# Kernel tuning notes

Hardware: AMD Instinct MI355X
Metric: run time of the kernel (lower is better)

## Reference

```python
import jax, jax.numpy as jnp
import numpy as np

NEG_SLOPE = 0.01  # torch leaky_relu default

def _leaky_relu(x):
    return jnp.where(x >= 0, x, NEG_SLOPE * x)

def setup_inputs() -> dict:
    key = jax.random.key(0)
    ks = jax.random.split(key, 12)
    n_drug, n_disease, n_edges, d = 10000, 10000, 1000000, 100
    inp = {
        "x_drug": jax.random.normal(ks[0], (n_drug, d), dtype=jnp.float32),
        "x_disease": jax.random.normal(ks[1], (n_disease, d), dtype=jnp.float32),
        "edge_label_index": jax.random.randint(ks[2], (2, n_edges), 0, n_drug, dtype=jnp.int64),
        "W1": jax.random.normal(ks[3], (200, 128), dtype=jnp.float32) * 0.07,
        "b1": jax.random.normal(ks[4], (128,), dtype=jnp.float32) * 0.01,
        "W2": jax.random.normal(ks[5], (128, 32), dtype=jnp.float32) * 0.09,
        "b2": jax.random.normal(ks[6], (32,), dtype=jnp.float32) * 0.01,
        "W3": jax.random.normal(ks[7], (32, 16), dtype=jnp.float32) * 0.18,
        "b3": jax.random.normal(ks[8], (16,), dtype=jnp.float32) * 0.01,
        "W4": jax.random.normal(ks[9], (16, 1), dtype=jnp.float32) * 0.25,
        "b4": jax.random.normal(ks[10], (1,), dtype=jnp.float32) * 0.01,
    }
    return inp

def reference(x_drug, x_disease, edge_label_index, W1, b1, W2, b2, W3, b3, W4, b4):
    # gather per-edge node embeddings and concat -> [E, 200]
    ef = jnp.concatenate([x_drug[edge_label_index[0]],
                          x_disease[edge_label_index[1]]], axis=-1)
    ef = _leaky_relu(ef @ W1 + b1)
    ef = _leaky_relu(ef @ W2 + b2)
    ef = _leaky_relu(ef @ W3 + b3)
    ef = ef @ W4 + b4
    return jnp.squeeze(ef, axis=-1)
```

## Files before the change

### kernel.cpp

```cpp
#include <hip/hip_runtime.h>
#include <cstdint>
#include <cstddef>

typedef _Float16 hf2   __attribute__((ext_vector_type(2)));
typedef _Float16 f16x8 __attribute__((ext_vector_type(8)));
typedef float    f32x4 __attribute__((ext_vector_type(4)));

__device__ __forceinline__ f16x8 q2h8(uint4 q) { union { uint4 q; f16x8 h; } c; c.q = q; return c.h; }
__device__ __forceinline__ hf2 pkrtz(float lo, float hi) {
    auto v = __builtin_amdgcn_cvt_pkrtz(lo, hi);
    union { decltype(v) a; hf2 b; } c; c.a = v; return c.b;
}
__device__ __forceinline__ float lreluf(float x) { return fmaxf(x, 0.01f * x); }
__device__ __forceinline__ f16x8 lrelu8(uint4 a, uint4 b) {
    f16x8 s = q2h8(a) + q2h8(b);
    f16x8 m = s * (_Float16)0.01f;
    return __builtin_elementwise_max(s, m);
}

__global__ __launch_bounds__(256) void node_proj2(
    const float* __restrict__ xd, const float* __restrict__ xi,
    const float* __restrict__ W1, const float* __restrict__ b1,
    _Float16* __restrict__ Pd, _Float16* __restrict__ Pi,
    int nd, int ni, int nblk_d, int nblk_i,
    const float* __restrict__ W2, const float* __restrict__ W3,
    _Float16* __restrict__ W2f, _Float16* __restrict__ W3f,
    const unsigned* __restrict__ ew, long long nwords, int* __restrict__ flag)
{
    const int t = threadIdx.x;
    const int nproj = nblk_d + nblk_i;

    if ((int)blockIdx.x >= nproj) {
        if ((int)blockIdx.x == nproj) {
            for (int idx = t; idx < 4096; idx += 256) {
                int i  = idx & 7;
                int l  = (idx >> 3) & 63;
                int kt = (idx >> 9) & 3;
                int nt = (idx >> 11) & 1;
                int k = kt * 32 + 8 * (l >> 4) + i;
                int j = nt * 16 + (l & 15);
                W2f[idx] = (_Float16)W2[k * 32 + j];
            }
            for (int idx = t; idx < 512; idx += 256) {
                int i = idx & 7, l = idx >> 3;
                W3f[idx] = (_Float16)W3[(8 * (l >> 4) + i) * 16 + (l & 15)];
            }
        } else if (t < 64) {
            const long long pairs = nwords / 2;
            const long long step  = pairs / 64;
            unsigned v = 0;
            for (int s = 0; s < 4; ++s) {
                long long p = (long long)t * step + (long long)s * (step / 4 + 1);
                if (p < pairs) v |= ew[2 * p + 1];
            }
            unsigned long long ball = __ballot(v != 0);
            if (t == 0) *flag = (ball == 0ULL) ? 1 : 0;
        }
        return;
    }

    __shared__ float xs[1600];
    const int c  = t & 127;
    const int ty = t >> 7;
    const bool dis = (int)blockIdx.x >= nblk_d;
    const int b = dis ? (blockIdx.x - nblk_d) : blockIdx.x;
    const int n = dis ? ni : nd;
    const float* x = dis ? xi : xd;
    const float* W = dis ? (W1 + 100 * 128) : W1;
    _Float16* P = dis ? Pi : Pd;
    const float bv = dis ? b1[c] : 0.f;
    const int r0 = b * 16;

    const long long gbase = (long long)r0 * 100;
    const long long lim   = (long long)n * 100;
    for (int idx = t; idx < 1600; idx += 256) {
        long long g = gbase + idx;
        xs[idx] = (g < lim) ? x[g] : 0.f;
    }
    __syncthreads();

    float acc[8];
#pragma unroll
    for (int i = 0; i < 8; ++i) acc[i] = bv;

    const float4* xs4 = (const float4*)xs;
#pragma unroll 5
    for (int kk = 0; kk < 25; ++kk) {
        float w0 = W[(4 * kk + 0) * 128 + c];
        float w1 = W[(4 * kk + 1) * 128 + c];
        float w2 = W[(4 * kk + 2) * 128 + c];
        float w3 = W[(4 * kk + 3) * 128 + c];
#pragma unroll
        for (int i = 0; i < 8; ++i) {
            float4 xv = xs4[(ty * 8 + i) * 25 + kk];
            acc[i] = fmaf(xv.x, w0, acc[i]);
            acc[i] = fmaf(xv.y, w1, acc[i]);
            acc[i] = fmaf(xv.z, w2, acc[i]);
            acc[i] = fmaf(xv.w, w3, acc[i]);
        }
    }
#pragma unroll
    for (int i = 0; i < 8; ++i) {
        int r = r0 + ty * 8 + i;
        if (r < n) P[(size_t)r * 128 + c] = (_Float16)acc[i];
    }
}

__global__ __launch_bounds__(64, 4) void edge_mlp(
    const void* __restrict__ eidx_raw,
    const _Float16* __restrict__ Pd, const _Float16* __restrict__ Pi,
    const _Float16* __restrict__ W2f, const float* __restrict__ b2,
    const _Float16* __restrict__ W3f, const float* __restrict__ b3,
    const float* __restrict__ W4, const float* __restrict__ b4,
    const int* __restrict__ flag64,
    float* __restrict__ out, int E)
{
    __shared__ __align__(16) float H2[64 * 36];

    const int l  = threadIdx.x;
    const int er = l & 15;
    const int cg = l >> 4;
    const int base = blockIdx.x * 64;
    const int e_c = min(base + l, E - 1);

    int i0, i1;
    if (*flag64) {
        const long long* p = (const long long*)eidx_raw;
        i0 = (int)p[e_c];
        i1 = (int)p[(size_t)E + e_c];
    } else {
        const int* p = (const int*)eidx_raw;
        i0 = p[e_c];
        i1 = p[(size_t)E + e_c];
    }

    f16x8 bf0[4], bf1[4];
    {
        const uint4* W2q = (const uint4*)W2f;
#pragma unroll
        for (int kt = 0; kt < 4; ++kt) {
            bf0[kt] = q2h8(W2q[kt * 64 + l]);
            bf1[kt] = q2h8(W2q[256 + kt * 64 + l]);
        }
    }
    const f16x8 w3f = q2h8(((const uint4*)W3f)[l]);
    const float  b2v0 = b2[er], b2v1 = b2[16 + er];
    const float4 b3q  = ((const float4*)b3)[cg];
    const float4 w4q  = ((const float4*)W4)[cg];
    const float  b4v  = b4[0];

#pragma unroll
    for (int q = 0; q < 4; ++q) {
        const int src = q * 16 + er;
        const int j0 = __shfl(i0, src, 64);
        const int j1 = __shfl(i1, src, 64);
        const uint4* rowD = (const uint4*)(Pd + (size_t)j0 * 128);
        const uint4* rowI = (const uint4*)(Pi + (size_t)j1 * 128);

        f32x4 c0 = {0.f, 0.f, 0.f, 0.f}, c1 = {0.f, 0.f, 0.f, 0.f};
#pragma unroll
        for (int kt = 0; kt < 4; ++kt) {
            f16x8 af = lrelu8(rowD[kt * 4 + cg], rowI[kt * 4 + cg]);
            c0 = __builtin_amdgcn_mfma_f32_16x16x32_f16(af, bf0[kt], c0, 0, 0, 0);
            c1 = __builtin_amdgcn_mfma_f32_16x16x32_f16(af, bf1[kt], c1, 0, 0, 0);
        }

#pragma unroll
        for (int r = 0; r < 4; ++r) {
            const int e = q * 16 + 4 * cg + r;
            H2[e * 36 + er]      = lreluf(c0[r] + b2v0);
            H2[e * 36 + 16 + er] = lreluf(c1[r] + b2v1);
        }
        __syncthreads();

        const int e2 = q * 16 + er;
        const float4* hr = (const float4*)&H2[e2 * 36 + 8 * cg];
        float4 h0 = hr[0], h1 = hr[1];
        union { hf2 h[4]; f16x8 v; } u;
        u.h[0] = pkrtz(h0.x, h0.y);
        u.h[1] = pkrtz(h0.z, h0.w);
        u.h[2] = pkrtz(h1.x, h1.y);
        u.h[3] = pkrtz(h1.z, h1.w);

        f32x4 d3 = __builtin_amdgcn_mfma_f32_16x16x32_f16(
            w3f, u.v, (f32x4){0.f, 0.f, 0.f, 0.f}, 0, 0, 0);

        float v = lreluf(d3[0] + b3q.x) * w4q.x;
        v      += lreluf(d3[1] + b3q.y) * w4q.y;
        v      += lreluf(d3[2] + b3q.z) * w4q.z;
        v      += lreluf(d3[3] + b3q.w) * w4q.w;
        v += __shfl_xor(v, 16, 64);
        v += __shfl_xor(v, 32, 64);

        if (cg == 0) {
            const int eo = base + q * 16 + er;
            if (eo < E) out[eo] = v + b4v;
        }
        __syncthreads();
    }
}

extern "C" void kernel_launch(void* const* d_in, const int* in_sizes, int n_in,
                              void* d_out, int out_size, void* d_ws, size_t ws_size,
                              hipStream_t stream)
{
    const float* x_drug = (const float*)d_in[0];
    const float* x_dis  = (const float*)d_in[1];
    const void*  eidx   = d_in[2];
    const float* W1 = (const float*)d_in[3];
    const float* b1 = (const float*)d_in[4];
    const float* W2 = (const float*)d_in[5];
    const float* b2 = (const float*)d_in[6];
    const float* W3 = (const float*)d_in[7];
    const float* b3 = (const float*)d_in[8];
    const float* W4 = (const float*)d_in[9];
    const float* b4 = (const float*)d_in[10];

    const int nd = in_sizes[0] / 100;
    const int ni = in_sizes[1] / 100;
    const int E  = in_sizes[2] / 2;

    char* ws = (char*)d_ws;
    _Float16* Pd  = (_Float16*)ws;                   size_t off = (size_t)nd * 128 * 2;
    _Float16* Pi  = (_Float16*)(ws + off);           off += (size_t)ni * 128 * 2;
    _Float16* W2f = (_Float16*)(ws + off);           off += 4096 * 2;
    _Float16* W3f = (_Float16*)(ws + off);           off += 512 * 2;
    int* flag = (int*)(ws + off);

    const int nblk_d = (nd + 15) / 16;
    const int nblk_i = (ni + 15) / 16;

    node_proj2<<<nblk_d + nblk_i + 2, 256, 0, stream>>>(
        x_drug, x_dis, W1, b1, Pd, Pi, nd, ni, nblk_d, nblk_i,
        W2, W3, W2f, W3f,
        (const unsigned*)eidx, 2LL * E, flag);

    edge_mlp<<<(E + 63) / 64, 64, 0, stream>>>(eidx, Pd, Pi,
                                               W2f, b2, W3f, b3, W4, b4,
                                               flag, (float*)d_out, E);
}
```

Before: 161.4 us.

## Batch all edge-row gathers per wave and drop block barriers in edge MLP

The edge kernel now runs 256-thread blocks, with each wave owning a private shared-memory tile. All four 16-edge gather+MFMA groups are issued before any layer-2 activations are written, and the per-iteration __syncthreads are removed because waves only touch their own tile. This exposes more outstanding gather loads per wave and removes barrier stalls. In exchange it raises register pressure by keeping eight accumulators live, and it drops the launch_bounds occupancy hint.

```diff
diff --git a/kernel.cpp b/kernel.cpp
--- a/kernel.cpp
+++ b/kernel.cpp
@@ -106,7 +106,7 @@
     }
 }
 
-__global__ __launch_bounds__(64, 4) void edge_mlp(
+__global__ __launch_bounds__(256) void edge_mlp(
     const void* __restrict__ eidx_raw,
     const _Float16* __restrict__ Pd, const _Float16* __restrict__ Pi,
     const _Float16* __restrict__ W2f, const float* __restrict__ b2,
@@ -115,13 +115,16 @@
     const int* __restrict__ flag64,
     float* __restrict__ out, int E)
 {
-    __shared__ __align__(16) float H2[64 * 36];
-
-    const int l  = threadIdx.x;
+    __shared__ __align__(16) float H2[4][64 * 36];
+
+    const int t  = threadIdx.x;
+    const int l  = t & 63;
+    const int w  = t >> 6;
     const int er = l & 15;
     const int cg = l >> 4;
-    const int base = blockIdx.x * 64;
+    const int base = blockIdx.x * 256 + w * 64;
     const int e_c = min(base + l, E - 1);
+    float* Hw = H2[w];
 
     int i0, i1;
     if (*flag64) {
@@ -149,6 +152,7 @@
     const float4 w4q  = ((const float4*)W4)[cg];
     const float  b4v  = b4[0];
 
+    f32x4 c0[4], c1[4];
 #pragma unroll
     for (int q = 0; q < 4; ++q) {
         const int src = q * 16 + er;
@@ -156,25 +160,29 @@
         const int j1 = __shfl(i1, src, 64);
         const uint4* rowD = (const uint4*)(Pd + (size_t)j0 * 128);
         const uint4* rowI = (const uint4*)(Pi + (size_t)j1 * 128);
-
-        f32x4 c0 = {0.f, 0.f, 0.f, 0.f}, c1 = {0.f, 0.f, 0.f, 0.f};
+        c0[q] = (f32x4){0.f, 0.f, 0.f, 0.f};
+        c1[q] = (f32x4){0.f, 0.f, 0.f, 0.f};
 #pragma unroll
         for (int kt = 0; kt < 4; ++kt) {
             f16x8 af = lrelu8(rowD[kt * 4 + cg], rowI[kt * 4 + cg]);
-            c0 = __builtin_amdgcn_mfma_f32_16x16x32_f16(af, bf0[kt], c0, 0, 0, 0);
-            c1 = __builtin_amdgcn_mfma_f32_16x16x32_f16(af, bf1[kt], c1, 0, 0, 0);
-        }
-
+            c0[q] = __builtin_amdgcn_mfma_f32_16x16x32_f16(af, bf0[kt], c0[q], 0, 0, 0);
+            c1[q] = __builtin_amdgcn_mfma_f32_16x16x32_f16(af, bf1[kt], c1[q], 0, 0, 0);
+        }
+    }
+
+#pragma unroll
+    for (int q = 0; q < 4; ++q)
 #pragma unroll
         for (int r = 0; r < 4; ++r) {
             const int e = q * 16 + 4 * cg + r;
-            H2[e * 36 + er]      = lreluf(c0[r] + b2v0);
-            H2[e * 36 + 16 + er] = lreluf(c1[r] + b2v1);
-        }
-        __syncthreads();
-
+            Hw[e * 36 + er]      = lreluf(c0[q][r] + b2v0);
+            Hw[e * 36 + 16 + er] = lreluf(c1[q][r] + b2v1);
+        }
+
+#pragma unroll
+    for (int q = 0; q < 4; ++q) {
         const int e2 = q * 16 + er;
-        const float4* hr = (const float4*)&H2[e2 * 36 + 8 * cg];
+        const float4* hr = (const float4*)&Hw[e2 * 36 + 8 * cg];
         float4 h0 = hr[0], h1 = hr[1];
         union { hf2 h[4]; f16x8 v; } u;
         u.h[0] = pkrtz(h0.x, h0.y);
@@ -196,7 +204,6 @@
             const int eo = base + q * 16 + er;
             if (eo < E) out[eo] = v + b4v;
         }
-        __syncthreads();
     }
 }
 
@@ -235,7 +242,7 @@
         W2, W3, W2f, W3f,
         (const unsigned*)eidx, 2LL * E, flag);
 
-    edge_mlp<<<(E + 63) / 64, 64, 0, stream>>>(eidx, Pd, Pi,
-                                               W2f, b2, W3f, b3, W4, b4,
-                                               flag, (float*)d_out, E);
-}
+    edge_mlp<<<(E + 255) / 256, 256, 0, stream>>>(eidx, Pd, Pi,
+                                                  W2f, b2, W3f, b3, W4, b4,
+                                                  flag, (float*)d_out, E);
+}
```

Result: no change. 162.9 us (+0.9%).

## Split edge MLP to one 16-edge tile per wave with batched gathers

Applied to the files above, without the earlier changes.

The edge kernel now uses 512-thread blocks in which each wave handles a single 16-edge tile, replacing one wave looping over four tiles. Each lane issues all eight gather loads for its drug and disease rows up front with inline-asm global_load_dwordx4 and a single vmcnt wait, to raise memory-level parallelism on the latency-bound gather. W2 and W3 fragments are staged once per block in LDS instead of read from global memory by every wave. The layer-2 activations go through a per-wave f16 LDS scratch with no block barriers. The costs are the LDS weight staging and one block-wide barrier per block.

```diff
diff --git a/kernel.cpp b/kernel.cpp
--- a/kernel.cpp
+++ b/kernel.cpp
@@ -5,18 +5,23 @@
 typedef _Float16 hf2   __attribute__((ext_vector_type(2)));
 typedef _Float16 f16x8 __attribute__((ext_vector_type(8)));
 typedef float    f32x4 __attribute__((ext_vector_type(4)));
-
-__device__ __forceinline__ f16x8 q2h8(uint4 q) { union { uint4 q; f16x8 h; } c; c.q = q; return c.h; }
+typedef unsigned int u32x4 __attribute__((ext_vector_type(4)));
+
+__device__ __forceinline__ f16x8 b2h8(u32x4 q) { union { u32x4 q; f16x8 h; } c; c.q = q; return c.h; }
 __device__ __forceinline__ hf2 pkrtz(float lo, float hi) {
     auto v = __builtin_amdgcn_cvt_pkrtz(lo, hi);
     union { decltype(v) a; hf2 b; } c; c.a = v; return c.b;
 }
 __device__ __forceinline__ float lreluf(float x) { return fmaxf(x, 0.01f * x); }
-__device__ __forceinline__ f16x8 lrelu8(uint4 a, uint4 b) {
-    f16x8 s = q2h8(a) + q2h8(b);
+__device__ __forceinline__ f16x8 lrelu8(u32x4 a, u32x4 b) {
+    f16x8 s = b2h8(a) + b2h8(b);
     f16x8 m = s * (_Float16)0.01f;
     return __builtin_elementwise_max(s, m);
 }
+
+#define GLOAD(dst, ptr, off) \
+    asm volatile("global_load_dwordx4 %0, %1, off offset:" #off \
+                 : "=v"(dst) : "v"(ptr) : "memory")
 
 __global__ __launch_bounds__(256) void node_proj2(
     const float* __restrict__ xd, const float* __restrict__ xi,
@@ -106,7 +111,7 @@
     }
 }
 
-__global__ __launch_bounds__(64, 4) void edge_mlp(
+__global__ __launch_bounds__(512, 4) void edge_mlp(
     const void* __restrict__ eidx_raw,
     const _Float16* __restrict__ Pd, const _Float16* __restrict__ Pi,
     const _Float16* __restrict__ W2f, const float* __restrict__ b2,
@@ -115,14 +120,20 @@
     const int* __restrict__ flag64,
     float* __restrict__ out, int E)
 {
-    __shared__ __align__(16) float H2[64 * 36];
-
-    const int l  = threadIdx.x;
+    __shared__ __align__(16) u32x4 Ws[1216];
+
+    const int t  = threadIdx.x;
+    const int l  = t & 63;
+    const int w  = t >> 6;
     const int er = l & 15;
     const int cg = l >> 4;
-    const int base = blockIdx.x * 64;
-    const int e_c = min(base + l, E - 1);
-
+    const int base = blockIdx.x * 128 + w * 16;
+
+    Ws[t] = ((const u32x4*)W2f)[t];
+    if (t < 64) Ws[512 + t] = ((const u32x4*)W3f)[t];
+    __syncthreads();
+
+    const int e_c = min(base + er, E - 1);
     int i0, i1;
     if (*flag64) {
         const long long* p = (const long long*)eidx_raw;
@@ -135,68 +146,71 @@
     }
 
     f16x8 bf0[4], bf1[4];
-    {
-        const uint4* W2q = (const uint4*)W2f;
-#pragma unroll
-        for (int kt = 0; kt < 4; ++kt) {
-            bf0[kt] = q2h8(W2q[kt * 64 + l]);
-            bf1[kt] = q2h8(W2q[256 + kt * 64 + l]);
-        }
-    }
-    const f16x8 w3f = q2h8(((const uint4*)W3f)[l]);
+#pragma unroll
+    for (int kt = 0; kt < 4; ++kt) {
+        bf0[kt] = b2h8(Ws[kt * 64 + l]);
+        bf1[kt] = b2h8(Ws[256 + kt * 64 + l]);
+    }
+    const f16x8 w3f = b2h8(Ws[512 + l]);
+    _Float16* Hw = (_Float16*)&Ws[576 + w * 80];
+
     const float  b2v0 = b2[er], b2v1 = b2[16 + er];
     const float4 b3q  = ((const float4*)b3)[cg];
     const float4 w4q  = ((const float4*)W4)[cg];
     const float  b4v  = b4[0];
 
-#pragma unroll
-    for (int q = 0; q < 4; ++q) {
-        const int src = q * 16 + er;
-        const int j0 = __shfl(i0, src, 64);
-        const int j1 = __shfl(i1, src, 64);
-        const uint4* rowD = (const uint4*)(Pd + (size_t)j0 * 128);
-        const uint4* rowI = (const uint4*)(Pi + (size_t)j1 * 128);
-
-        f32x4 c0 = {0.f, 0.f, 0.f, 0.f}, c1 = {0.f, 0.f, 0.f, 0.f};
-#pragma unroll
-        for (int kt = 0; kt < 4; ++kt) {
-            f16x8 af = lrelu8(rowD[kt * 4 + cg], rowI[kt * 4 + cg]);
-            c0 = __builtin_amdgcn_mfma_f32_16x16x32_f16(af, bf0[kt], c0, 0, 0, 0);
-            c1 = __builtin_amdgcn_mfma_f32_16x16x32_f16(af, bf1[kt], c1, 0, 0, 0);
-        }
-
-#pragma unroll
-        for (int r = 0; r < 4; ++r) {
-            const int e = q * 16 + 4 * cg + r;
-            H2[e * 36 + er]      = lreluf(c0[r] + b2v0);
-            H2[e * 36 + 16 + er] = lreluf(c1[r] + b2v1);
-        }
-        __syncthreads();
-
-        const int e2 = q * 16 + er;
-        const float4* hr = (const float4*)&H2[e2 * 36 + 8 * cg];
-        float4 h0 = hr[0], h1 = hr[1];
-        union { hf2 h[4]; f16x8 v; } u;
-        u.h[0] = pkrtz(h0.x, h0.y);
-        u.h[1] = pkrtz(h0.z, h0.w);
-        u.h[2] = pkrtz(h1.x, h1.y);
-        u.h[3] = pkrtz(h1.z, h1.w);
-
-        f32x4 d3 = __builtin_amdgcn_mfma_f32_16x16x32_f16(
-            w3f, u.v, (f32x4){0.f, 0.f, 0.f, 0.f}, 0, 0, 0);
-
-        float v = lreluf(d3[0] + b3q.x) * w4q.x;
-        v      += lreluf(d3[1] + b3q.y) * w4q.y;
-        v      += lreluf(d3[2] + b3q.z) * w4q.z;
-        v      += lreluf(d3[3] + b3q.w) * w4q.w;
-        v += __shfl_xor(v, 16, 64);
-        v += __shfl_xor(v, 32, 64);
-
-        if (cg == 0) {
-            const int eo = base + q * 16 + er;
-            if (eo < E) out[eo] = v + b4v;
-        }
-        __syncthreads();
+    const char* pD = (const char*)(Pd + (size_t)i0 * 128) + cg * 16;
+    const char* pI = (const char*)(Pi + (size_t)i1 * 128) + cg * 16;
+    u32x4 a0, a1, a2, a3, v0, v1, v2, v3;
+    GLOAD(a0, pD, 0);
+    GLOAD(a1, pD, 64);
+    GLOAD(a2, pD, 128);
+    GLOAD(a3, pD, 192);
+    GLOAD(v0, pI, 0);
+    GLOAD(v1, pI, 64);
+    GLOAD(v2, pI, 128);
+    GLOAD(v3, pI, 192);
+    asm volatile("s_waitcnt vmcnt(0)" ::: "memory");
+    __builtin_amdgcn_sched_barrier(0);
+
+    f32x4 c0 = {0.f, 0.f, 0.f, 0.f}, c1 = {0.f, 0.f, 0.f, 0.f};
+    {
+        f16x8 af;
+        af = lrelu8(a0, v0);
+        c0 = __builtin_amdgcn_mfma_f32_16x16x32_f16(af, bf0[0], c0, 0, 0, 0);
+        c1 = __builtin_amdgcn_mfma_f32_16x16x32_f16(af, bf1[0], c1, 0, 0, 0);
+        af = lrelu8(a1, v1);
+        c0 = __builtin_amdgcn_mfma_f32_16x16x32_f16(af, bf0[1], c0, 0, 0, 0);
+        c1 = __builtin_amdgcn_mfma_f32_16x16x32_f16(af, bf1[1], c1, 0, 0, 0);
+        af = lrelu8(a2, v2);
+        c0 = __builtin_amdgcn_mfma_f32_16x16x32_f16(af, bf0[2], c0, 0, 0, 0);
+        c1 = __builtin_amdgcn_mfma_f32_16x16x32_f16(af, bf1[2], c1, 0, 0, 0);
+        af = lrelu8(a3, v3);
+        c0 = __builtin_amdgcn_mfma_f32_16x16x32_f16(af, bf0[3], c0, 0, 0, 0);
+        c1 = __builtin_amdgcn_mfma_f32_16x16x32_f16(af, bf1[3], c1, 0, 0, 0);
+    }
+
+#pragma unroll
+    for (int r = 0; r < 4; ++r) {
+        const int e = 4 * cg + r;
+        Hw[e * 40 + er]      = (_Float16)lreluf(c0[r] + b2v0);
+        Hw[e * 40 + 16 + er] = (_Float16)lreluf(c1[r] + b2v1);
+    }
+
+    f16x8 hv = *(const f16x8*)&Hw[er * 40 + 8 * cg];
+    f32x4 d3 = __builtin_amdgcn_mfma_f32_16x16x32_f16(
+        w3f, hv, (f32x4){0.f, 0.f, 0.f, 0.f}, 0, 0, 0);
+
+    float v = lreluf(d3[0] + b3q.x) * w4q.x;
+    v      += lreluf(d3[1] + b3q.y) * w4q.y;
+    v      += lreluf(d3[2] + b3q.z) * w4q.z;
+    v      += lreluf(d3[3] + b3q.w) * w4q.w;
+    v += __shfl_xor(v, 16, 64);
+    v += __shfl_xor(v, 32, 64);
+
+    if (cg == 0) {
+        const int eo = base + er;
+        if (eo < E) out[eo] = v + b4v;
     }
 }
 
@@ -235,7 +249,7 @@
         W2, W3, W2f, W3f,
         (const unsigned*)eidx, 2LL * E, flag);
 
-    edge_mlp<<<(E + 63) / 64, 64, 0, stream>>>(eidx, Pd, Pi,
-                                               W2f, b2, W3f, b3, W4, b4,
-                                               flag, (float*)d_out, E);
-}
+    edge_mlp<<<(E + 127) / 128, 512, 0, stream>>>(eidx, Pd, Pi,
+                                                  W2f, b2, W3f, b3, W4, b4,
+                                                  flag, (float*)d_out, E);
+}
```

New measurement: 174.1 us. +7.9%, slower.
